# Kernel tuning notes

Hardware: AMD Instinct MI355X
Metric: run time of the kernel (lower is better)

Reference implementation:

```python
import jax, jax.numpy as jnp
import numpy as np

EPS = 1e-6  # cell eps
LN_EPS = 1e-5  # torch LayerNorm default


def layer_norm(x, gamma, beta):
    mu = jnp.mean(x, axis=-1, keepdims=True)
    var = jnp.mean(jnp.square(x - mu), axis=-1, keepdims=True)
    return (x - mu) * jax.lax.rsqrt(var + LN_EPS) * gamma + beta


def normalized_exp_gate(pre):
    centered = pre - jnp.mean(pre, axis=1, keepdims=True)
    e = jnp.exp(jnp.clip(centered, -5.0, 5.0))
    return e / (jnp.sum(e, axis=1, keepdims=True) + EPS)


def setup_inputs() -> dict:
    key = jax.random.key(0)
    B, Din, H = 8192, 512, 1024
    ks = jax.random.split(key, 16)
    std = 1.0 / np.sqrt(H)
    u = lambda k, shape: jax.random.uniform(k, shape, jnp.float32, -std, std)
    return {
        "x": jax.random.normal(ks[0], (B, Din), jnp.float32),
        "h_prev": jax.random.normal(ks[1], (B, H), jnp.float32),
        "c_prev": jax.random.normal(ks[2], (B, H), jnp.float32),
        "Wx": u(ks[3], (4 * H, Din)),
        "bx": u(ks[4], (4 * H,)),
        "Wh": u(ks[5], (4 * H, H)),
        "bh": u(ks[6], (4 * H,)),
        "ln_in_g": u(ks[7], (4 * H,)),
        "ln_in_b": u(ks[8], (4 * H,)),
        "ln_hu_g": u(ks[9], (4 * H,)),
        "ln_hu_b": u(ks[10], (4 * H,)),
        "ln_c_g": u(ks[11], (H,)),
        "ln_c_b": u(ks[12], (H,)),
        "ln_h_g": u(ks[13], (H,)),
        "ln_h_b": u(ks[14], (H,)),
    }


def reference(x, h_prev, c_prev, Wx, bx, Wh, bh,
              ln_in_g, ln_in_b, ln_hu_g, ln_hu_b,
              ln_c_g, ln_c_b, ln_h_g, ln_h_b):
    # dropout p=0 -> identity (eval mode)
    gates_x = layer_norm(x @ Wx.T + bx, ln_in_g, ln_in_b)      # [B, 4H]
    gates_h = layer_norm(h_prev @ Wh.T + bh, ln_hu_g, ln_hu_b)  # [B, 4H]
    gates = gates_x + gates_h
    i, f, g, o = jnp.split(gates, 4, axis=1)
    i = normalized_exp_gate(i)
    f = normalized_exp_gate(f)
    gate_sum = i + f
    i = i / (gate_sum + EPS)
    f = f / (gate_sum + EPS)
    c_tilde = jnp.tanh(g)
    c = layer_norm(f * c_prev + i * c_tilde, ln_c_g, ln_c_b)
    o = jax.nn.sigmoid(o)
    c_out = layer_norm(jnp.tanh(c), ln_h_g, ln_h_b)
    h = o * c_out
    return (h, c)
```

## Files before the change

### kernel.cpp

```cpp
#include <hip/hip_runtime.h>
#include <hip/hip_bf16.h>
#include <stdint.h>
#include <math.h>

#define EPS_CELL 1e-6f
#define LN_EPS   1e-5f

typedef short short8 __attribute__((ext_vector_type(8)));
typedef float f32x4 __attribute__((ext_vector_type(4)));
typedef unsigned short ushort;

__device__ __forceinline__ ushort f2bf(float f) {
    union { float f; uint32_t u; } v; v.f = f;
    uint32_t r = v.u + 0x7FFFu + ((v.u >> 16) & 1u);
    return (ushort)(r >> 16);
}
__device__ __forceinline__ float bfbits2f(uint32_t hi16_in_place) {
    union { uint32_t u; float f; } v; v.u = hi16_in_place;
    return v.f;
}

__global__ __launch_bounds__(256) void cast_f32_bf16(const float* __restrict__ in,
                                                     ushort* __restrict__ out,
                                                     int n) {
    int i = (blockIdx.x * 256 + threadIdx.x) * 8;
    if (i >= n) return;
    const float4* p = (const float4*)(in + i);
    float4 a = p[0], b = p[1];
    uint4 r;
    r.x = (uint32_t)f2bf(a.x) | ((uint32_t)f2bf(a.y) << 16);
    r.y = (uint32_t)f2bf(a.z) | ((uint32_t)f2bf(a.w) << 16);
    r.z = (uint32_t)f2bf(b.x) | ((uint32_t)f2bf(b.y) << 16);
    r.w = (uint32_t)f2bf(b.z) | ((uint32_t)f2bf(b.w) << 16);
    *(uint4*)(out + i) = r;
}

#define BAR()        __builtin_amdgcn_s_barrier()
#define SPRIO(x)     __builtin_amdgcn_s_setprio(x)
#define WAIT_LGKM0() do { asm volatile("s_waitcnt lgkmcnt(0)" ::: "memory"); \
                          __builtin_amdgcn_sched_barrier(0); } while (0)
#define WAIT_VM2()   do { asm volatile("s_waitcnt vmcnt(2)" ::: "memory"); \
                          __builtin_amdgcn_sched_barrier(0); } while (0)

template<int K>
__global__ __launch_bounds__(512, 2) void gemm256_8ph(
        const ushort* __restrict__ Ag,
        const ushort* __restrict__ Bg,
        const float*  __restrict__ bias,
        ushort* __restrict__ C,
        int M, int GN) {
    constexpr int NT = K / 64;
    constexpr int NP = NT / 2;

    __shared__ ushort lds[65536];

    const int t    = threadIdx.x;
    const int lane = t & 63;
    const int w    = t >> 6;
    const int wr   = w >> 2;
    const int wc   = w & 3;
    const int ln   = lane & 15;
    const int hi   = lane >> 4;
    const int sx   = ln & 7;

    const int bid = blockIdx.x;
    const int wg  = (bid & 7) * 64 + (bid >> 3);
    const int n0  = (wg & 15) * 256;
    const int m0  = (wg >> 4) * 256;

    const int trow = t >> 3;
    const int scol = (((t & 7) ^ (trow & 7)) * 8);

#define STG_A(buf, j, kb) __builtin_amdgcn_global_load_lds( \
    (const __attribute__((address_space(1))) void*)(Ag + (size_t)(m0 + (j)*64 + trow) * K + (kb) + scol), \
    (__attribute__((address_space(3))) void*)(lds + (buf)*32768 + (j)*4096 + t*8), 16, 0, 0)
#define STG_B(buf, j, kb) __builtin_amdgcn_global_load_lds( \
    (const __attribute__((address_space(1))) void*)(Bg + (size_t)(n0 + (j)*64 + trow) * K + (kb) + scol), \
    (__attribute__((address_space(3))) void*)(lds + (buf)*32768 + 16384 + (j)*4096 + t*8), 16, 0, 0)

    const int ca0  = ((0 + hi) ^ sx) * 8;
    const int ca1  = ((4 + hi) ^ sx) * 8;
    const int arow = (wr * 128 + ln) * 64;
    const int brow = (wc * 64 + ln) * 64;

    short8 af[2][4], bf0[2][2], bf1[2][2];
    f32x4  acc[8][4] = {};

#define LD_A(buf, mbase) do { _Pragma("unroll") for (int m = 0; m < 4; ++m) { \
    af[0][m] = *(const short8*)&lds[(buf)*32768 + arow + ((mbase)+m)*1024 + ca0]; \
    af[1][m] = *(const short8*)&lds[(buf)*32768 + arow + ((mbase)+m)*1024 + ca1]; } } while (0)
#define LD_B(dst, buf, nbase) do { _Pragma("unroll") for (int n = 0; n < 2; ++n) { \
    dst[0][n] = *(const short8*)&lds[(buf)*32768 + 16384 + brow + ((nbase)+n)*1024 + ca0]; \
    dst[1][n] = *(const short8*)&lds[(buf)*32768 + 16384 + brow + ((nbase)+n)*1024 + ca1]; } } while (0)
#define MMQ(mb, nb, B_) do { _Pragma("unroll") for (int kk = 0; kk < 2; ++kk) \
    _Pragma("unroll") for (int m = 0; m < 4; ++m) \
    _Pragma("unroll") for (int n = 0; n < 2; ++n) \
        acc[(mb)+m][(nb)+n] = __builtin_amdgcn_mfma_f32_16x16x32_bf16( \
            af[kk][m], B_[kk][n], acc[(mb)+m][(nb)+n], 0, 0, 0); } while (0)

    STG_B(0,0,0); STG_B(0,1,0); STG_B(0,2,0); STG_B(0,3,0);
    STG_A(0,0,0); STG_A(0,2,0); STG_A(0,1,0); STG_A(0,3,0);
    STG_B(1,0,64); STG_B(1,1,64);
    WAIT_VM2(); BAR();

    for (int p = 0; p < NP; ++p) {
        const int k1 = (2*p + 1) * 64;
        const int k2 = ((2*p + 2) & (NT - 1)) * 64;
        const int k3 = ((2*p + 3) & (NT - 1)) * 64;

        LD_A(0, 0); LD_B(bf0, 0, 0);
        STG_B(1,2,k1); STG_B(1,3,k1);
        BAR(); WAIT_LGKM0();
        SPRIO(1); MMQ(0,0,bf0); SPRIO(0); BAR();
        LD_B(bf1, 0, 2);
        STG_A(1,0,k1); STG_A(1,2,k1);
        BAR(); WAIT_LGKM0();
        SPRIO(1); MMQ(0,2,bf1); SPRIO(0); BAR();
        LD_A(0, 4);
        STG_A(1,1,k1); STG_A(1,3,k1);
        BAR(); WAIT_LGKM0();
        SPRIO(1); MMQ(4,0,bf0); SPRIO(0); BAR();
        STG_B(0,0,k2); STG_B(0,1,k2);
        BAR();
        SPRIO(1); MMQ(4,2,bf1); SPRIO(0);
        WAIT_VM2(); BAR();
        LD_A(1, 0); LD_B(bf0, 1, 0);
        STG_B(0,2,k2); STG_B(0,3,k2);
        BAR(); WAIT_LGKM0();
        SPRIO(1); MMQ(0,0,bf0); SPRIO(0); BAR();
        LD_B(bf1, 1, 2);
        STG_A(0,0,k2); STG_A(0,2,k2);
        BAR(); WAIT_LGKM0();
        SPRIO(1); MMQ(0,2,bf1); SPRIO(0); BAR();
        LD_A(1, 4);
        STG_A(0,1,k2); STG_A(0,3,k2);
        BAR(); WAIT_LGKM0();
        SPRIO(1); MMQ(4,0,bf0); SPRIO(0); BAR();
        STG_B(1,0,k3); STG_B(1,1,k3);
        BAR();
        SPRIO(1); MMQ(4,2,bf1); SPRIO(0);
        WAIT_VM2(); BAR();
    }

#pragma unroll
    for (int n = 0; n < 4; ++n) {
        int col  = n0 + wc * 64 + n * 16 + ln;
        float bv = bias[col];
#pragma unroll
        for (int m = 0; m < 8; ++m) {
            int row = m0 + wr * 128 + m * 16 + hi * 4;
#pragma unroll
            for (int r = 0; r < 4; ++r)
                C[(size_t)(row + r) * GN + col] = f2bf(acc[m][n][r] + bv);
        }
    }
#undef STG_A
#undef STG_B
#undef LD_A
#undef LD_B
#undef MMQ
}

template<int NV>
__device__ __forceinline__ void block_reduce_sum(float* v, float* sred) {
    const int lane = threadIdx.x & 63;
    const int w    = threadIdx.x >> 6;
#pragma unroll
    for (int i = 0; i < NV; ++i) {
        float s = v[i];
#pragma unroll
        for (int o = 32; o > 0; o >>= 1) s += __shfl_down(s, o, 64);
        if (lane == 0) sred[i * 4 + w] = s;
    }
    __syncthreads();
#pragma unroll
    for (int i = 0; i < NV; ++i)
        v[i] = sred[i * 4 + 0] + sred[i * 4 + 1] + sred[i * 4 + 2] + sred[i * 4 + 3];
    __syncthreads();
}

__global__ __launch_bounds__(256) void fused_cell(
        const ushort* __restrict__ U, const ushort* __restrict__ V,
        const float* __restrict__ c_prev,
        const float* __restrict__ g_in, const float* __restrict__ b_in,
        const float* __restrict__ g_hu, const float* __restrict__ b_hu,
        const float* __restrict__ g_c,  const float* __restrict__ b_c,
        const float* __restrict__ g_h,  const float* __restrict__ b_h,
        float* __restrict__ out_h, float* __restrict__ out_c) {
    __shared__ __align__(16) float sg[4096];
    __shared__ float sred[16];
    const int r = blockIdx.x;
    const int t = threadIdx.x;
    const size_t rowG = (size_t)r * 4096;
    const size_t rowH = (size_t)r * 1024;

    float uf[16], vf[16];
    {
        const uint4* pu = (const uint4*)(U + rowG + (size_t)t * 16);
        const uint4* pv = (const uint4*)(V + rowG + (size_t)t * 16);
        uint4 u0 = pu[0], u1 = pu[1], v0 = pv[0], v1 = pv[1];
        uint32_t uw[8] = {u0.x, u0.y, u0.z, u0.w, u1.x, u1.y, u1.z, u1.w};
        uint32_t vw[8] = {v0.x, v0.y, v0.z, v0.w, v1.x, v1.y, v1.z, v1.w};
#pragma unroll
        for (int j = 0; j < 8; ++j) {
            uf[2 * j]     = bfbits2f(uw[j] << 16);
            uf[2 * j + 1] = bfbits2f(uw[j] & 0xFFFF0000u);
            vf[2 * j]     = bfbits2f(vw[j] << 16);
            vf[2 * j + 1] = bfbits2f(vw[j] & 0xFFFF0000u);
        }
    }
    float red[4] = {0.f, 0.f, 0.f, 0.f};
#pragma unroll
    for (int j = 0; j < 16; ++j) {
        red[0] += uf[j]; red[1] += uf[j] * uf[j];
        red[2] += vf[j]; red[3] += vf[j] * vf[j];
    }
    block_reduce_sum<4>(red, sred);
    const float inv4096 = 1.f / 4096.f;
    float mu_u = red[0] * inv4096, mu_v = red[2] * inv4096;
    float rs_u = rsqrtf(red[1] * inv4096 - mu_u * mu_u + LN_EPS);
    float rs_v = rsqrtf(red[3] * inv4096 - mu_v * mu_v + LN_EPS);

#pragma unroll
    for (int j = 0; j < 16; ++j) {
        int idx = t * 16 + j;
        float zu = (uf[j] - mu_u) * rs_u;
        float zv = (vf[j] - mu_v) * rs_v;
        sg[idx] = zu * g_in[idx] + b_in[idx] + zv * g_hu[idx] + b_hu[idx];
    }
    __syncthreads();

    const float4* sg4 = (const float4*)sg;
    float4 gi4 = sg4[0 * 256 + t];
    float4 gf4 = sg4[1 * 256 + t];
    float4 gg4 = sg4[2 * 256 + t];
    float4 go4 = sg4[3 * 256 + t];
    float gi[4] = {gi4.x, gi4.y, gi4.z, gi4.w};
    float gf[4] = {gf4.x, gf4.y, gf4.z, gf4.w};
    float gg[4] = {gg4.x, gg4.y, gg4.z, gg4.w};
    float go[4] = {go4.x, go4.y, go4.z, go4.w};

    red[0] = gi[0] + gi[1] + gi[2] + gi[3];
    red[1] = gf[0] + gf[1] + gf[2] + gf[3];
    block_reduce_sum<2>(red, sred);
    const float inv1024 = 1.f / 1024.f;
    float mi = red[0] * inv1024, mf = red[1] * inv1024;

    float ei[4], ef[4];
#pragma unroll
    for (int q = 0; q < 4; ++q) {
        ei[q] = expf(fminf(fmaxf(gi[q] - mi, -5.f), 5.f));
        ef[q] = expf(fminf(fmaxf(gf[q] - mf, -5.f), 5.f));
    }
    red[0] = ei[0] + ei[1] + ei[2] + ei[3];
    red[1] = ef[0] + ef[1] + ef[2] + ef[3];
    block_reduce_sum<2>(red, sred);
    float inv_si = 1.f / (red[0] + EPS_CELL);
    float inv_sf = 1.f / (red[1] + EPS_CELL);

    const float4* cp4p = (const float4*)(c_prev + rowH);
    float4 cp4 = cp4p[t];
    float cprev[4] = {cp4.x, cp4.y, cp4.z, cp4.w};

    float cpv[4];
#pragma unroll
    for (int q = 0; q < 4; ++q) {
        float in_ = ei[q] * inv_si;
        float fn_ = ef[q] * inv_sf;
        float den = 1.f / (in_ + fn_ + EPS_CELL);
        float i2 = in_ * den, f2 = fn_ * den;
        cpv[q] = f2 * cprev[q] + i2 * tanhf(gg[q]);
    }
    red[0] = cpv[0] + cpv[1] + cpv[2] + cpv[3];
    red[1] = cpv[0] * cpv[0] + cpv[1] * cpv[1] + cpv[2] * cpv[2] + cpv[3] * cpv[3];
    block_reduce_sum<2>(red, sred);
    float mu_c = red[0] * inv1024;
    float rs_c = rsqrtf(red[1] * inv1024 - mu_c * mu_c + LN_EPS);

    float cv[4], th[4];
#pragma unroll
    for (int q = 0; q < 4; ++q) {
        int j = t * 4 + q;
        cv[q] = (cpv[q] - mu_c) * rs_c * g_c[j] + b_c[j];
        th[q] = tanhf(cv[q]);
    }
    {
        float4 o; o.x = cv[0]; o.y = cv[1]; o.z = cv[2]; o.w = cv[3];
        *(float4*)(out_c + rowH + (size_t)t * 4) = o;
    }
    red[0] = th[0] + th[1] + th[2] + th[3];
    red[1] = th[0] * th[0] + th[1] * th[1] + th[2] * th[2] + th[3] * th[3];
    block_reduce_sum<2>(red, sred);
    float mu_t = red[0] * inv1024;
    float rs_t = rsqrtf(red[1] * inv1024 - mu_t * mu_t + LN_EPS);

    float hv[4];
#pragma unroll
    for (int q = 0; q < 4; ++q) {
        int j = t * 4 + q;
        float co = (th[q] - mu_t) * rs_t * g_h[j] + b_h[j];
        float so = 1.f / (1.f + expf(-go[q]));
        hv[q] = so * co;
    }
    {
        float4 o; o.x = hv[0]; o.y = hv[1]; o.z = hv[2]; o.w = hv[3];
        *(float4*)(out_h + rowH + (size_t)t * 4) = o;
    }
}

extern "C" void kernel_launch(void* const* d_in, const int* in_sizes, int n_in,
                              void* d_out, int out_size, void* d_ws, size_t ws_size,
                              hipStream_t stream) {
    const float* x       = (const float*)d_in[0];
    const float* h_prev  = (const float*)d_in[1];
    const float* c_prev  = (const float*)d_in[2];
    const float* Wx      = (const float*)d_in[3];
    const float* bx      = (const float*)d_in[4];
    const float* Wh      = (const float*)d_in[5];
    const float* bh      = (const float*)d_in[6];
    const float* ln_in_g = (const float*)d_in[7];
    const float* ln_in_b = (const float*)d_in[8];
    const float* ln_hu_g = (const float*)d_in[9];
    const float* ln_hu_b = (const float*)d_in[10];
    const float* ln_c_g  = (const float*)d_in[11];
    const float* ln_c_b  = (const float*)d_in[12];
    const float* ln_h_g  = (const float*)d_in[13];
    const float* ln_h_b  = (const float*)d_in[14];

    const int B = 8192, Din = 512, H = 1024, G = 4096;

    ushort* xb  = (ushort*)d_ws;
    ushort* hb  = xb  + (size_t)B * Din;
    ushort* wxb = hb  + (size_t)B * H;
    ushort* whb = wxb + (size_t)G * Din;
    ushort* U   = whb + (size_t)G * H;
    ushort* V   = U   + (size_t)B * G;

    cast_f32_bf16<<<(B * Din) / 2048, 256, 0, stream>>>(x, xb, B * Din);
    cast_f32_bf16<<<(B * H)   / 2048, 256, 0, stream>>>(h_prev, hb, B * H);
    cast_f32_bf16<<<(G * Din) / 2048, 256, 0, stream>>>(Wx, wxb, G * Din);
    cast_f32_bf16<<<(G * H)   / 2048, 256, 0, stream>>>(Wh, whb, G * H);

    gemm256_8ph<512> <<<dim3(512), 512, 0, stream>>>(xb, wxb, bx, U, B, G);
    gemm256_8ph<1024><<<dim3(512), 512, 0, stream>>>(hb, whb, bh, V, B, G);

    float* out_h = (float*)d_out;
    float* out_c = out_h + (size_t)B * H;
    fused_cell<<<B, 256, 0, stream>>>(U, V, c_prev,
                                      ln_in_g, ln_in_b, ln_hu_g, ln_hu_b,
                                      ln_c_g, ln_c_b, ln_h_g, ln_h_b,
                                      out_h, out_c);
}
```

Measured before the change: 246.4 us.

## Restage GEMM global loads and stage bf16 epilogue through swizzled LDS

The GEMM main loop now issues all four A-tile loads together and all four B-tile loads together, instead of interleaving half-tile loads across the phases. The wait threshold changes from vmcnt(2) to vmcnt(4), and the wrap-around tile indices are clamped rather than masked. The epilogue writes the bf16 results into LDS with an XOR swizzle, then emits coalesced 16-byte row stores to global memory instead of scattered 2-byte stores. This is meant to cut store transactions and smooth out global-load latency, at the cost of an extra LDS round trip and barriers.

```diff
diff --git a/kernel.cpp b/kernel.cpp
--- a/kernel.cpp
+++ b/kernel.cpp
@@ -39,7 +39,9 @@
 #define SPRIO(x)     __builtin_amdgcn_s_setprio(x)
 #define WAIT_LGKM0() do { asm volatile("s_waitcnt lgkmcnt(0)" ::: "memory"); \
                           __builtin_amdgcn_sched_barrier(0); } while (0)
-#define WAIT_VM2()   do { asm volatile("s_waitcnt vmcnt(2)" ::: "memory"); \
+#define WAIT_VM4()   do { asm volatile("s_waitcnt vmcnt(4)" ::: "memory"); \
+                          __builtin_amdgcn_sched_barrier(0); } while (0)
+#define WAIT_VM0()   do { asm volatile("s_waitcnt vmcnt(0)" ::: "memory"); \
                           __builtin_amdgcn_sched_barrier(0); } while (0)
 
 template<int K>
@@ -99,59 +101,72 @@
             af[kk][m], B_[kk][n], acc[(mb)+m][(nb)+n], 0, 0, 0); } while (0)
 
     STG_B(0,0,0); STG_B(0,1,0); STG_B(0,2,0); STG_B(0,3,0);
-    STG_A(0,0,0); STG_A(0,2,0); STG_A(0,1,0); STG_A(0,3,0);
-    STG_B(1,0,64); STG_B(1,1,64);
-    WAIT_VM2(); BAR();
+    STG_A(0,0,0); STG_A(0,1,0); STG_A(0,2,0); STG_A(0,3,0);
+    STG_B(1,0,64); STG_B(1,1,64); STG_B(1,2,64); STG_B(1,3,64);
+    WAIT_VM4(); BAR();
 
     for (int p = 0; p < NP; ++p) {
         const int k1 = (2*p + 1) * 64;
-        const int k2 = ((2*p + 2) & (NT - 1)) * 64;
-        const int k3 = ((2*p + 3) & (NT - 1)) * 64;
+        const int t2 = (2*p + 2 < NT) ? (2*p + 2) : (2*p);
+        const int t3 = (2*p + 3 < NT) ? (2*p + 3) : (2*p + 1);
+        const int k2 = t2 * 64, k3 = t3 * 64;
 
         LD_A(0, 0); LD_B(bf0, 0, 0);
-        STG_B(1,2,k1); STG_B(1,3,k1);
+        STG_A(1,0,k1); STG_A(1,1,k1); STG_A(1,2,k1); STG_A(1,3,k1);
         BAR(); WAIT_LGKM0();
         SPRIO(1); MMQ(0,0,bf0); SPRIO(0); BAR();
         LD_B(bf1, 0, 2);
-        STG_A(1,0,k1); STG_A(1,2,k1);
         BAR(); WAIT_LGKM0();
         SPRIO(1); MMQ(0,2,bf1); SPRIO(0); BAR();
         LD_A(0, 4);
-        STG_A(1,1,k1); STG_A(1,3,k1);
         BAR(); WAIT_LGKM0();
         SPRIO(1); MMQ(4,0,bf0); SPRIO(0); BAR();
-        STG_B(0,0,k2); STG_B(0,1,k2);
+        STG_B(0,0,k2); STG_B(0,1,k2); STG_B(0,2,k2); STG_B(0,3,k2);
         BAR();
         SPRIO(1); MMQ(4,2,bf1); SPRIO(0);
-        WAIT_VM2(); BAR();
+        WAIT_VM4(); BAR();
         LD_A(1, 0); LD_B(bf0, 1, 0);
-        STG_B(0,2,k2); STG_B(0,3,k2);
+        STG_A(0,0,k2); STG_A(0,1,k2); STG_A(0,2,k2); STG_A(0,3,k2);
         BAR(); WAIT_LGKM0();
         SPRIO(1); MMQ(0,0,bf0); SPRIO(0); BAR();
         LD_B(bf1, 1, 2);
-        STG_A(0,0,k2); STG_A(0,2,k2);
         BAR(); WAIT_LGKM0();
         SPRIO(1); MMQ(0,2,bf1); SPRIO(0); BAR();
         LD_A(1, 4);
-        STG_A(0,1,k2); STG_A(0,3,k2);
         BAR(); WAIT_LGKM0();
         SPRIO(1); MMQ(4,0,bf0); SPRIO(0); BAR();
-        STG_B(1,0,k3); STG_B(1,1,k3);
+        STG_B(1,0,k3); STG_B(1,1,k3); STG_B(1,2,k3); STG_B(1,3,k3);
         BAR();
         SPRIO(1); MMQ(4,2,bf1); SPRIO(0);
-        WAIT_VM2(); BAR();
-    }
-
+        WAIT_VM4(); BAR();
+    }
+
+    WAIT_VM0();
+    BAR();
 #pragma unroll
     for (int n = 0; n < 4; ++n) {
-        int col  = n0 + wc * 64 + n * 16 + ln;
-        float bv = bias[col];
+        int cl   = wc * 64 + n * 16 + ln;
+        float bv = bias[n0 + cl];
 #pragma unroll
         for (int m = 0; m < 8; ++m) {
-            int row = m0 + wr * 128 + m * 16 + hi * 4;
-#pragma unroll
-            for (int r = 0; r < 4; ++r)
-                C[(size_t)(row + r) * GN + col] = f2bf(acc[m][n][r] + bv);
+#pragma unroll
+            for (int r = 0; r < 4; ++r) {
+                int row = wr * 128 + m * 16 + hi * 4 + r;
+                int sc  = (cl & 7) + ((((cl >> 3) ^ (row & 7))) << 3);
+                lds[row * 256 + sc] = f2bf(acc[m][n][r] + bv);
+            }
+        }
+    }
+    BAR();
+    {
+        const int rr = t >> 5;
+        const int oc = (t & 31) * 8;
+#pragma unroll
+        for (int i = 0; i < 16; ++i) {
+            int row = i * 16 + rr;
+            int sc  = (((oc >> 3) ^ (row & 7)) << 3);
+            uint4 vv = *(const uint4*)&lds[row * 256 + sc];
+            *(uint4*)(C + (size_t)(m0 + row) * GN + n0 + oc) = vv;
         }
     }
 #undef STG_A
```

Result: no change. 246.7 us (+0.1%).
